# Kernel tuning notes

Measured on AMD Instinct MI355X. Metric: run time of the kernel, lower is better.

## Reference

```python
import jax, jax.numpy as jnp
import numpy as np

# MoE config (mirrors init_kwargs)
E = 8        # num_experts
K = 2        # num_experts_per_tok
H = 1024     # hidden_size
F = 2816     # moe_intermediate_size
B, S = 2, 512
NORM_TOPK = True


def setup_inputs() -> dict:
    key = jax.random.key(0)
    ks = jax.random.split(key, 5)
    x = jax.random.normal(ks[0], (B, S, H), dtype=jnp.float32)
    router_w = jax.random.normal(ks[1], (E, H), dtype=jnp.float32) * 0.02   # nn.Linear(H, E).weight
    gate_proj = jax.random.normal(ks[2], (E, H, F), dtype=jnp.float32) * 0.02
    up_proj = jax.random.normal(ks[3], (E, H, F), dtype=jnp.float32) * 0.02
    down_proj = jax.random.normal(ks[4], (E, F, H), dtype=jnp.float32) * 0.02
    return {"x": x, "router_w": router_w, "gate_proj": gate_proj,
            "up_proj": up_proj, "down_proj": down_proj}


def reference(x, router_w, gate_proj, up_proj, down_proj):
    b, s, h = x.shape
    xf = x.reshape(-1, h)                                    # [T, H]
    # Router: softmax over experts, top-k selection mask
    logits = xf @ router_w.T                                 # [T, E]
    probs = jax.nn.softmax(logits, axis=-1)
    topk_p, topk_i = jax.lax.top_k(probs, K)                 # [T, K]
    routing_map = jax.nn.one_hot(topk_i, E, dtype=probs.dtype).sum(axis=1)  # [T, E] 0/1
    if NORM_TOPK:
        probs = probs / topk_p.sum(-1, keepdims=True)
    weight = probs * routing_map                             # [T, E]; zero for unselected experts
    # Per-expert SwiGLU FFN; combine weighted by routing prob.
    # Dense-masked formulation: mathematically identical to the original
    # gather -> per-expert GEMM -> scatter_add, since weight==0 for unrouted pairs.
    g = jnp.einsum('th,ehf->tef', xf, gate_proj)             # [T, E, F]
    u = jnp.einsum('th,ehf->tef', xf, up_proj)               # [T, E, F]
    m = jax.nn.silu(g) * u                                   # [T, E, F]
    out = jnp.einsum('tef,efh,te->th', m, down_proj, weight) # [T, H]
    return out.reshape(b, s, h)
```

## Files before the change

kernel.cpp:

```cpp
#include <hip/hip_runtime.h>

#define HD 1024
#define FD 2816
#define NE 8
#define NT 1024
#define NSLOT (NT * 2)

typedef short short8 __attribute__((ext_vector_type(8)));
typedef short short4v __attribute__((ext_vector_type(4)));
typedef unsigned u32x4 __attribute__((ext_vector_type(4)));
typedef unsigned u32x2 __attribute__((ext_vector_type(2)));
typedef float f32x4 __attribute__((ext_vector_type(4)));
typedef float f32x16 __attribute__((ext_vector_type(16)));

typedef __attribute__((address_space(3))) unsigned lds_u32;
typedef __attribute__((address_space(1))) const unsigned glb_u32;

#define WAITV(N) asm volatile("s_waitcnt vmcnt(" #N ") lgkmcnt(0)" ::: "memory")
#define BARRIER() do { __builtin_amdgcn_s_barrier(); __builtin_amdgcn_sched_barrier(0); } while (0)

__device__ __forceinline__ void glds16(const void* g, void* l) {
  __builtin_amdgcn_global_load_lds((glb_u32*)g, (lds_u32*)l, 16, 0, 0);
}

__device__ __forceinline__ short f2bf(float f) {
  unsigned u = __builtin_bit_cast(unsigned, f);
  u += 0x7FFFu + ((u >> 16) & 1u);
  return (short)(u >> 16);
}

__device__ __forceinline__ unsigned cvtpk(float lo, float hi) {
  unsigned r;
  asm("v_cvt_pk_bf16_f32 %0, %1, %2" : "=v"(r) : "v"(lo), "v"(hi));
  return r;
}
__device__ __forceinline__ int imin(int a, int b) { return a < b ? a : b; }

__global__ void router_kernel(const float* __restrict__ x,
                              const float* __restrict__ rw,
                              int* __restrict__ counts,
                              int* __restrict__ tok_i,
                              float* __restrict__ tok_w) {
  const int t = blockIdx.x;
  const int lane = threadIdx.x;
  const float* px = x + (size_t)t * HD;
  float acc[NE];
#pragma unroll
  for (int e = 0; e < NE; e++) acc[e] = 0.f;
  for (int h = lane; h < HD; h += 64) {
    float xv = px[h];
#pragma unroll
    for (int e = 0; e < NE; e++) acc[e] += xv * rw[e * HD + h];
  }
#pragma unroll
  for (int e = 0; e < NE; e++) {
#pragma unroll
    for (int off = 32; off > 0; off >>= 1)
      acc[e] += __shfl_xor(acc[e], off, 64);
  }
  if (lane == 0) {
    float mx = acc[0];
#pragma unroll
    for (int e = 1; e < NE; e++) mx = fmaxf(mx, acc[e]);
    float ex[NE];
#pragma unroll
    for (int e = 0; e < NE; e++) ex[e] = __expf(acc[e] - mx);
    int i1 = 0;
#pragma unroll
    for (int e = 1; e < NE; e++) if (ex[e] > ex[i1]) i1 = e;
    int i2 = (i1 == 0) ? 1 : 0;
#pragma unroll
    for (int e = 0; e < NE; e++) if (e != i1 && ex[e] > ex[i2]) i2 = e;
    float inv = 1.f / (ex[i1] + ex[i2]);
    tok_i[t * 2 + 0] = i1; tok_w[t * 2 + 0] = ex[i1] * inv;
    tok_i[t * 2 + 1] = i2; tok_w[t * 2 + 1] = ex[i2] * inv;
    atomicAdd(&counts[i1], 1);
    atomicAdd(&counts[i2], 1);
  }
}

__global__ void scan_kernel(const int* __restrict__ counts,
                            int* __restrict__ bases,
                            int* __restrict__ cursor) {
  if (threadIdx.x == 0) {
    int s = 0;
    for (int e = 0; e < NE; e++) { bases[e] = s; cursor[e] = s; s += counts[e]; }
    bases[NE] = s;
  }
}

__global__ void fill_kernel(const int* __restrict__ tok_i,
                            const float* __restrict__ tok_w,
                            int* __restrict__ cursor,
                            int* __restrict__ slot_token,
                            float* __restrict__ slot_w,
                            int* __restrict__ slot_of) {
  int t = blockIdx.x * 256 + threadIdx.x;
  if (t >= NT) return;
#pragma unroll
  for (int k = 0; k < 2; k++) {
    int e = tok_i[t * 2 + k];
    int pos = atomicAdd(&cursor[e], 1);
    slot_token[pos] = t;
    slot_w[pos] = tok_w[t * 2 + k];
    slot_of[t * 2 + k] = pos;
  }
}

__global__ void gather_kernel(const float* __restrict__ x,
                              const int* __restrict__ slot_token,
                              short* __restrict__ xg) {
  const int slot = blockIdx.x;
  const int tok = slot_token[slot];
  const int t = threadIdx.x;
  f32x4 v = *(const f32x4*)(x + (size_t)tok * HD + t * 4);
  u32x2 s;
  s[0] = cvtpk(v[0], v[1]);
  s[1] = cvtpk(v[2], v[3]);
  *(u32x2*)&xg[(size_t)slot * HD + t * 4] = s;
}


#define GU_STAGEA(buf, k0) do {                                    \
    glds16(asrc[0] + (k0), &As[buf][wid * 512]);                   \
    glds16(asrc[1] + (k0), &As[buf][2048 + wid * 512]);            \
  } while (0)

#define GU_LOADB(G, U, k0) do {                                    \
    _Pragma("unroll")                                              \
    for (int ks = 0; ks < 2; ks++) {                               \
      _Pragma("unroll")                                            \
      for (int j = 0; j < 8; j++) {                                \
        unsigned idx = lidx + (unsigned)((k0) + ks * 16 + j) * FD; \
        G[ks * 8 + j] = Gw[idx];                                   \
        U[ks * 8 + j] = Uw[idx];                                   \
      }                                                            \
    }                                                              \
  } while (0)

#define GU_COMPUTE(Ab, G, U) do {                                             \
    _Pragma("unroll")                                                         \
    for (int ks = 0; ks < 2; ks++) {                                          \
      const int oct = ks * 2 + l5;                                            \
      short8 a0, a1;                                                          \
      { int r = wm * 64 + l31, p = r >> 1;                                    \
        a0 = *(const short8*)((Ab) + p * 64 +                                 \
              ((((r & 1) << 2) | oct) ^ (p & 7)) * 8); }                      \
      { int r = wm * 64 + 32 + l31, p = r >> 1;                               \
        a1 = *(const short8*)((Ab) + p * 64 +                                 \
              ((((r & 1) << 2) | oct) ^ (p & 7)) * 8); }                      \
      u32x4 ug, uu;                                                           \
      _Pragma("unroll")                                                       \
      for (int t2 = 0; t2 < 4; t2++) {                                        \
        ug[t2] = cvtpk(G[ks * 8 + 2 * t2], G[ks * 8 + 2 * t2 + 1]);           \
        uu[t2] = cvtpk(U[ks * 8 + 2 * t2], U[ks * 8 + 2 * t2 + 1]);           \
      }                                                                       \
      short8 bg = __builtin_bit_cast(short8, ug);                             \
      short8 bu = __builtin_bit_cast(short8, uu);                             \
      accG0 = __builtin_amdgcn_mfma_f32_32x32x16_bf16(a0, bg, accG0, 0, 0, 0);\
      accU0 = __builtin_amdgcn_mfma_f32_32x32x16_bf16(a0, bu, accU0, 0, 0, 0);\
      accG1 = __builtin_amdgcn_mfma_f32_32x32x16_bf16(a1, bg, accG1, 0, 0, 0);\
      accU1 = __builtin_amdgcn_mfma_f32_32x32x16_bf16(a1, bu, accU1, 0, 0, 0);\
    }                                                                         \
  } while (0)

__global__ __launch_bounds__(256, 2) void gateup_kernel(
    const short* __restrict__ xg, const float* __restrict__ gate_w,
    const float* __restrict__ up_w, const int* __restrict__ bases,
    short* __restrict__ m_out) {
  const int bx = blockIdx.x;
  const int e = bx / 44, nt = bx - e * 44;
  const int b0 = bases[e];
  const int ne = bases[e + 1] - b0;
  const int row0 = blockIdx.y * 128;
  if (row0 >= ne) return;
  const int n0 = nt * 64;

  __shared__ short As[2][4096];

  const int tid = threadIdx.x;
  const int lane = tid & 63, wid = tid >> 6;
  const int l31 = lane & 31, l5 = lane >> 5;
  const int wm = wid >> 1, wn = wid & 1;

  const short* asrc[2];
#pragma unroll
  for (int q = 0; q < 2; q++) {
    int i = q * 256 + tid;
    int p = i >> 3, j = i & 7;
    int v = j ^ (p & 7);
    int r = 2 * p + (v >> 2), c = v & 3;
    int slot = b0 + imin(row0 + r, ne - 1);
    asrc[q] = xg + (size_t)slot * HD + c * 8;
  }

  const float* Gw = gate_w + (size_t)e * HD * FD;
  const float* Uw = up_w + (size_t)e * HD * FD;
  const unsigned lidx = (unsigned)(l5 * 8) * FD + n0 + wn * 32 + l31;

  f32x16 accG0 = (f32x16)0.f, accG1 = (f32x16)0.f;
  f32x16 accU0 = (f32x16)0.f, accU1 = (f32x16)0.f;
  f32x16 bvAG, bvAU, bvBG, bvBU;

  GU_STAGEA(0, 0);
  __builtin_amdgcn_sched_barrier(0);
  GU_LOADB(bvAG, bvAU, 0);
  WAITV(32); BARRIER();

  for (int t = 0; t < 32; t += 2) {
    GU_STAGEA(1, (t + 1) * 32);
    __builtin_amdgcn_sched_barrier(0);
    GU_LOADB(bvBG, bvBU, (t + 1) * 32);
    GU_COMPUTE(&As[0][0], bvAG, bvAU);
    WAITV(32); BARRIER();
    if (t + 2 < 32) {
      GU_STAGEA(0, (t + 2) * 32);
      __builtin_amdgcn_sched_barrier(0);
      GU_LOADB(bvAG, bvAU, (t + 2) * 32);
      GU_COMPUTE(&As[1][0], bvBG, bvBU);
      WAITV(32); BARRIER();
    } else {
      GU_COMPUTE(&As[1][0], bvBG, bvBU);
    }
  }

#pragma unroll
  for (int q = 0; q < 16; q++) {
    int rb_ = (q & 3) + 8 * (q >> 2) + 4 * l5;
    {
      int r = row0 + wm * 64 + rb_;
      if (r < ne) {
        int slot = b0 + r;
        float g = accG0[q], u = accU0[q];
        float mv = (g / (1.f + __expf(-g))) * u;
        m_out[(size_t)slot * FD + n0 + wn * 32 + l31] = f2bf(mv);
      }
    }
    {
      int r = row0 + wm * 64 + 32 + rb_;
      if (r < ne) {
        int slot = b0 + r;
        float g = accG1[q], u = accU1[q];
        float mv = (g / (1.f + __expf(-g))) * u;
        m_out[(size_t)slot * FD + n0 + wn * 32 + l31] = f2bf(mv);
      }
    }
  }
}


#define DW_STAGEA(buf, k0) do {                                    \
    glds16(asrc[0] + (k0), &As[buf][wid * 512]);                   \
    glds16(asrc[1] + (k0), &As[buf][2048 + wid * 512]);            \
  } while (0)

#define DW_LOADB(B0, B1, k0) do {                                  \
    _Pragma("unroll")                                              \
    for (int ks = 0; ks < 4; ks++) {                               \
      _Pragma("unroll")                                            \
      for (int j = 0; j < 8; j++) {                                \
        unsigned idx = lidx + (unsigned)((k0) + ks * 16 + j) * HD; \
        if (ks < 2) B0[ks * 8 + j] = Dw[idx];                      \
        else        B1[(ks - 2) * 8 + j] = Dw[idx];                \
      }                                                            \
    }                                                              \
  } while (0)

#define DW_COMPUTE(Ab, B0, B1) do {                                           \
    _Pragma("unroll")                                                         \
    for (int ks = 0; ks < 4; ks++) {                                          \
      const int sub = ks >> 1, oct = (ks & 1) * 2 + l5;                       \
      int r = wm * 32 + l31, p = r >> 1;                                      \
      short8 a = *(const short8*)((Ab) + sub * 2048 + p * 64 +                \
                  ((((r & 1) << 2) | oct) ^ (p & 7)) * 8);                    \
      u32x4 ub;                                                               \
      _Pragma("unroll")                                                       \
      for (int t2 = 0; t2 < 4; t2++) {                                        \
        if (ks < 2)                                                           \
          ub[t2] = cvtpk(B0[ks * 8 + 2 * t2], B0[ks * 8 + 2 * t2 + 1]);       \
        else                                                                  \
          ub[t2] = cvtpk(B1[(ks - 2) * 8 + 2 * t2],                           \
                         B1[(ks - 2) * 8 + 2 * t2 + 1]);                      \
      }                                                                       \
      short8 bf = __builtin_bit_cast(short8, ub);                             \
      acc = __builtin_amdgcn_mfma_f32_32x32x16_bf16(a, bf, acc, 0, 0, 0);     \
    }                                                                         \
  } while (0)

__global__ __launch_bounds__(256, 3) void down_kernel(
    const short* __restrict__ m_in, const float* __restrict__ dw,
    const int* __restrict__ bases, const float* __restrict__ slot_w,
    float* __restrict__ out_slot) {
  const int bx = blockIdx.x;
  const int e = bx >> 4, nt = bx & 15;
  const int b0 = bases[e];
  const int ne = bases[e + 1] - b0;
  const int row0 = blockIdx.y * 64;
  if (row0 >= ne) return;
  const int n0 = nt * 64;

  __shared__ short As[2][4096];

  const int tid = threadIdx.x;
  const int lane = tid & 63, wid = tid >> 6;
  const int l31 = lane & 31, l5 = lane >> 5;
  const int wm = wid >> 1, wn = wid & 1;

  const short* asrc[2];
#pragma unroll
  for (int q = 0; q < 2; q++) {
    int i = q * 256 + tid;
    int sub = i >> 8, ci = i & 255;
    int p = ci >> 3, j = ci & 7;
    int v = j ^ (p & 7);
    int r = 2 * p + (v >> 2), c = v & 3;
    int slot = b0 + imin(row0 + r, ne - 1);
    asrc[q] = m_in + (size_t)slot * FD + sub * 32 + c * 8;
  }

  const float* Dw = dw + (size_t)e * FD * HD;
  const unsigned lidx = (unsigned)(l5 * 8) * HD + n0 + wn * 32 + l31;

  f32x16 acc = (f32x16)0.f;
  f32x16 bvA0, bvA1, bvB0, bvB1;

  DW_STAGEA(0, 0);
  __builtin_amdgcn_sched_barrier(0);
  DW_LOADB(bvA0, bvA1, 0);
  WAITV(32); BARRIER();

  const int NTL = FD / 64;
  for (int t = 0; t < NTL; t += 2) {
    DW_STAGEA(1, (t + 1) * 64);
    __builtin_amdgcn_sched_barrier(0);
    DW_LOADB(bvB0, bvB1, (t + 1) * 64);
    DW_COMPUTE(&As[0][0], bvA0, bvA1);
    WAITV(32); BARRIER();
    if (t + 2 < NTL) {
      DW_STAGEA(0, (t + 2) * 64);
      __builtin_amdgcn_sched_barrier(0);
      DW_LOADB(bvA0, bvA1, (t + 2) * 64);
      DW_COMPUTE(&As[1][0], bvB0, bvB1);
      WAITV(32); BARRIER();
    } else {
      DW_COMPUTE(&As[1][0], bvB0, bvB1);
    }
  }

#pragma unroll
  for (int q = 0; q < 16; q++) {
    int r = row0 + wm * 32 + (q & 3) + 8 * (q >> 2) + 4 * l5;
    if (r < ne) {
      int slot = b0 + r;
      out_slot[(size_t)slot * HD + n0 + wn * 32 + l31] = acc[q] * slot_w[slot];
    }
  }
}

__global__ void combine_kernel(const float* __restrict__ out_slot,
                               const int* __restrict__ slot_of,
                               float* __restrict__ out) {
  const int t = blockIdx.x;
  const int s0 = slot_of[t * 2];
  const int s1 = slot_of[t * 2 + 1];
  const int i = threadIdx.x * 4;
  f32x4 a = *(const f32x4*)(out_slot + (size_t)s0 * HD + i);
  f32x4 b = *(const f32x4*)(out_slot + (size_t)s1 * HD + i);
  f32x4 c = a + b;
  *(f32x4*)(out + (size_t)t * HD + i) = c;
}

extern "C" void kernel_launch(void* const* d_in, const int* in_sizes, int n_in,
                              void* d_out, int out_size, void* d_ws,
                              size_t ws_size, hipStream_t stream) {
  const float* x = (const float*)d_in[0];
  const float* rw = (const float*)d_in[1];
  const float* gw = (const float*)d_in[2];
  const float* uw = (const float*)d_in[3];
  const float* dw = (const float*)d_in[4];
  float* out = (float*)d_out;

  char* ws = (char*)d_ws;
  int* counts = (int*)(ws + 0);
  int* cursor = (int*)(ws + 64);
  int* bases = (int*)(ws + 128);
  int* tok_i = (int*)(ws + 256);
  float* tok_w = (float*)(ws + 8448);
  int* slot_token = (int*)(ws + 16640);
  float* slot_w = (float*)(ws + 24832);
  int* slot_of = (int*)(ws + 33024);
  short* xg = (short*)(ws + 41216);
  short* m_buf = (short*)(ws + 4235520);
  float* out_slot = (float*)(ws + 15769856);

  (void)hipMemsetAsync(counts, 0, 64, stream);
  router_kernel<<<NT, 64, 0, stream>>>(x, rw, counts, tok_i, tok_w);
  scan_kernel<<<1, 64, 0, stream>>>(counts, bases, cursor);
  fill_kernel<<<NT / 256, 256, 0, stream>>>(tok_i, tok_w, cursor, slot_token,
                                            slot_w, slot_of);
  gather_kernel<<<NSLOT, 256, 0, stream>>>(x, slot_token, xg);
  gateup_kernel<<<dim3(352, 16), 256, 0, stream>>>(xg, gw, uw, bases, m_buf);
  down_kernel<<<dim3(128, 32), 256, 0, stream>>>(m_buf, dw, bases, slot_w,
                                                 out_slot);
  combine_kernel<<<NT, 256, 0, stream>>>(out_slot, slot_of, out);
}
```

Before: 214.6 us.

## Deepen gate-up and down GEMM pipelines to three-stage prefetch

Both the gate/up and down GEMM kernels move from a double-buffered loop to a triple-buffered one, with three LDS A-stages and three register sets for B. Loads for step t+3 are issued right after computing step t, and the vmcnt waits are relaxed so more global loads stay in flight. The down kernel also cuts its K step from 64 to 32, which halves the per-stage LDS and register footprint. The cost is more live registers in gate/up (six f32x16 B buffers), which could cause spills or lower occupancy, and more barriers per unit of K in the down kernel.

```diff
diff --git a/kernel.cpp b/kernel.cpp
--- a/kernel.cpp
+++ b/kernel.cpp
@@ -7,7 +7,6 @@
 #define NSLOT (NT * 2)
 
 typedef short short8 __attribute__((ext_vector_type(8)));
-typedef short short4v __attribute__((ext_vector_type(4)));
 typedef unsigned u32x4 __attribute__((ext_vector_type(4)));
 typedef unsigned u32x2 __attribute__((ext_vector_type(2)));
 typedef float f32x4 __attribute__((ext_vector_type(4)));
@@ -18,6 +17,7 @@
 
 #define WAITV(N) asm volatile("s_waitcnt vmcnt(" #N ") lgkmcnt(0)" ::: "memory")
 #define BARRIER() do { __builtin_amdgcn_s_barrier(); __builtin_amdgcn_sched_barrier(0); } while (0)
+#define SB() __builtin_amdgcn_sched_barrier(0)
 
 __device__ __forceinline__ void glds16(const void* g, void* l) {
   __builtin_amdgcn_global_load_lds((glb_u32*)g, (lds_u32*)l, 16, 0, 0);
@@ -121,9 +121,9 @@
 }
 
 
-#define GU_STAGEA(buf, k0) do {                                    \
-    glds16(asrc[0] + (k0), &As[buf][wid * 512]);                   \
-    glds16(asrc[1] + (k0), &As[buf][2048 + wid * 512]);            \
+#define GU_STAGEA(S, koff) do {                                    \
+    glds16(asrc[0] + (koff), &As[S][wid * 512]);                   \
+    glds16(asrc[1] + (koff), &As[S][2048 + wid * 512]);            \
   } while (0)
 
 #define GU_LOADB(G, U, k0) do {                                    \
@@ -164,6 +164,16 @@
     }                                                                         \
   } while (0)
 
+#define GU_ITER(S, T) do {                       \
+    GU_COMPUTE(&As[S][0], bG##S, bU##S);         \
+    BARRIER();                                   \
+    GU_STAGEA(S, ((T) + 3) * 32);                \
+    SB();                                        \
+    GU_LOADB(bG##S, bU##S, ((T) + 3) * 32);      \
+    WAITV(63);                                   \
+    BARRIER();                                   \
+  } while (0)
+
 __global__ __launch_bounds__(256, 2) void gateup_kernel(
     const short* __restrict__ xg, const float* __restrict__ gate_w,
     const float* __restrict__ up_w, const int* __restrict__ bases,
@@ -176,7 +186,7 @@
   if (row0 >= ne) return;
   const int n0 = nt * 64;
 
-  __shared__ short As[2][4096];
+  __shared__ short As[3][4096];
 
   const int tid = threadIdx.x;
   const int lane = tid & 63, wid = tid >> 6;
@@ -200,29 +210,26 @@
 
   f32x16 accG0 = (f32x16)0.f, accG1 = (f32x16)0.f;
   f32x16 accU0 = (f32x16)0.f, accU1 = (f32x16)0.f;
-  f32x16 bvAG, bvAU, bvBG, bvBU;
-
-  GU_STAGEA(0, 0);
-  __builtin_amdgcn_sched_barrier(0);
-  GU_LOADB(bvAG, bvAU, 0);
-  WAITV(32); BARRIER();
-
-  for (int t = 0; t < 32; t += 2) {
-    GU_STAGEA(1, (t + 1) * 32);
-    __builtin_amdgcn_sched_barrier(0);
-    GU_LOADB(bvBG, bvBU, (t + 1) * 32);
-    GU_COMPUTE(&As[0][0], bvAG, bvAU);
-    WAITV(32); BARRIER();
-    if (t + 2 < 32) {
-      GU_STAGEA(0, (t + 2) * 32);
-      __builtin_amdgcn_sched_barrier(0);
-      GU_LOADB(bvAG, bvAU, (t + 2) * 32);
-      GU_COMPUTE(&As[1][0], bvBG, bvBU);
-      WAITV(32); BARRIER();
-    } else {
-      GU_COMPUTE(&As[1][0], bvBG, bvBU);
-    }
-  }
+  f32x16 bG0, bU0, bG1, bU1, bG2, bU2;
+
+  GU_STAGEA(0, 0);  SB(); GU_LOADB(bG0, bU0, 0);  SB();
+  GU_STAGEA(1, 32); SB(); GU_LOADB(bG1, bU1, 32); SB();
+  GU_STAGEA(2, 64); SB(); GU_LOADB(bG2, bU2, 64);
+  WAITV(63);
+  BARRIER();
+
+  for (int t = 0; t < 27; t += 3) {
+    GU_ITER(0, t);
+    GU_ITER(1, t + 1);
+    GU_ITER(2, t + 2);
+  }
+  GU_ITER(0, 27);
+  GU_ITER(1, 28);
+  GU_COMPUTE(&As[2][0], bG2, bU2);
+  WAITV(34); BARRIER();
+  GU_COMPUTE(&As[0][0], bG0, bU0);
+  WAITV(0); BARRIER();
+  GU_COMPUTE(&As[1][0], bG1, bU1);
 
 #pragma unroll
   for (int q = 0; q < 16; q++) {
@@ -249,42 +256,43 @@
 }
 
 
-#define DW_STAGEA(buf, k0) do {                                    \
-    glds16(asrc[0] + (k0), &As[buf][wid * 512]);                   \
-    glds16(asrc[1] + (k0), &As[buf][2048 + wid * 512]);            \
-  } while (0)
-
-#define DW_LOADB(B0, B1, k0) do {                                  \
+#define DW_STAGEA(S, koff) glds16(asrc + (koff), &As[S][wid * 512])
+
+#define DW_LOADB(B, k0) do {                                       \
     _Pragma("unroll")                                              \
-    for (int ks = 0; ks < 4; ks++) {                               \
+    for (int ks = 0; ks < 2; ks++) {                               \
       _Pragma("unroll")                                            \
       for (int j = 0; j < 8; j++) {                                \
         unsigned idx = lidx + (unsigned)((k0) + ks * 16 + j) * HD; \
-        if (ks < 2) B0[ks * 8 + j] = Dw[idx];                      \
-        else        B1[(ks - 2) * 8 + j] = Dw[idx];                \
+        B[ks * 8 + j] = Dw[idx];                                   \
       }                                                            \
     }                                                              \
   } while (0)
 
-#define DW_COMPUTE(Ab, B0, B1) do {                                           \
+#define DW_COMPUTE(Ab, B) do {                                                \
     _Pragma("unroll")                                                         \
-    for (int ks = 0; ks < 4; ks++) {                                          \
-      const int sub = ks >> 1, oct = (ks & 1) * 2 + l5;                       \
+    for (int ks = 0; ks < 2; ks++) {                                          \
+      const int oct = ks * 2 + l5;                                            \
       int r = wm * 32 + l31, p = r >> 1;                                      \
-      short8 a = *(const short8*)((Ab) + sub * 2048 + p * 64 +                \
+      short8 a = *(const short8*)((Ab) + p * 64 +                             \
                   ((((r & 1) << 2) | oct) ^ (p & 7)) * 8);                    \
       u32x4 ub;                                                               \
       _Pragma("unroll")                                                       \
-      for (int t2 = 0; t2 < 4; t2++) {                                        \
-        if (ks < 2)                                                           \
-          ub[t2] = cvtpk(B0[ks * 8 + 2 * t2], B0[ks * 8 + 2 * t2 + 1]);       \
-        else                                                                  \
-          ub[t2] = cvtpk(B1[(ks - 2) * 8 + 2 * t2],                           \
-                         B1[(ks - 2) * 8 + 2 * t2 + 1]);                      \
-      }                                                                       \
+      for (int t2 = 0; t2 < 4; t2++)                                          \
+        ub[t2] = cvtpk(B[ks * 8 + 2 * t2], B[ks * 8 + 2 * t2 + 1]);           \
       short8 bf = __builtin_bit_cast(short8, ub);                             \
       acc = __builtin_amdgcn_mfma_f32_32x32x16_bf16(a, bf, acc, 0, 0, 0);     \
     }                                                                         \
+  } while (0)
+
+#define DW_ITER(S, T) do {                       \
+    DW_COMPUTE(&As[S][0], bv##S);                \
+    BARRIER();                                   \
+    DW_STAGEA(S, ((T) + 3) * 32);                \
+    SB();                                        \
+    DW_LOADB(bv##S, ((T) + 3) * 32);             \
+    WAITV(34);                                   \
+    BARRIER();                                   \
   } while (0)
 
 __global__ __launch_bounds__(256, 3) void down_kernel(
@@ -299,53 +307,45 @@
   if (row0 >= ne) return;
   const int n0 = nt * 64;
 
-  __shared__ short As[2][4096];
+  __shared__ short As[3][2048];
 
   const int tid = threadIdx.x;
   const int lane = tid & 63, wid = tid >> 6;
   const int l31 = lane & 31, l5 = lane >> 5;
   const int wm = wid >> 1, wn = wid & 1;
 
-  const short* asrc[2];
-#pragma unroll
-  for (int q = 0; q < 2; q++) {
-    int i = q * 256 + tid;
-    int sub = i >> 8, ci = i & 255;
-    int p = ci >> 3, j = ci & 7;
+  const short* asrc;
+  {
+    int p = tid >> 3, j = tid & 7;
     int v = j ^ (p & 7);
     int r = 2 * p + (v >> 2), c = v & 3;
     int slot = b0 + imin(row0 + r, ne - 1);
-    asrc[q] = m_in + (size_t)slot * FD + sub * 32 + c * 8;
+    asrc = m_in + (size_t)slot * FD + c * 8;
   }
 
   const float* Dw = dw + (size_t)e * FD * HD;
   const unsigned lidx = (unsigned)(l5 * 8) * HD + n0 + wn * 32 + l31;
 
   f32x16 acc = (f32x16)0.f;
-  f32x16 bvA0, bvA1, bvB0, bvB1;
-
-  DW_STAGEA(0, 0);
-  __builtin_amdgcn_sched_barrier(0);
-  DW_LOADB(bvA0, bvA1, 0);
-  WAITV(32); BARRIER();
-
-  const int NTL = FD / 64;
-  for (int t = 0; t < NTL; t += 2) {
-    DW_STAGEA(1, (t + 1) * 64);
-    __builtin_amdgcn_sched_barrier(0);
-    DW_LOADB(bvB0, bvB1, (t + 1) * 64);
-    DW_COMPUTE(&As[0][0], bvA0, bvA1);
-    WAITV(32); BARRIER();
-    if (t + 2 < NTL) {
-      DW_STAGEA(0, (t + 2) * 64);
-      __builtin_amdgcn_sched_barrier(0);
-      DW_LOADB(bvA0, bvA1, (t + 2) * 64);
-      DW_COMPUTE(&As[1][0], bvB0, bvB1);
-      WAITV(32); BARRIER();
-    } else {
-      DW_COMPUTE(&As[1][0], bvB0, bvB1);
-    }
-  }
+  f32x16 bv0, bv1, bv2;
+
+  DW_STAGEA(0, 0);  SB(); DW_LOADB(bv0, 0);  SB();
+  DW_STAGEA(1, 32); SB(); DW_LOADB(bv1, 32); SB();
+  DW_STAGEA(2, 64); SB(); DW_LOADB(bv2, 64);
+  WAITV(34);
+  BARRIER();
+
+  for (int t = 0; t < 84; t += 3) {
+    DW_ITER(0, t);
+    DW_ITER(1, t + 1);
+    DW_ITER(2, t + 2);
+  }
+  DW_ITER(0, 84);
+  DW_COMPUTE(&As[1][0], bv1);
+  WAITV(17); BARRIER();
+  DW_COMPUTE(&As[2][0], bv2);
+  WAITV(0); BARRIER();
+  DW_COMPUTE(&As[0][0], bv0);
 
 #pragma unroll
   for (int q = 0; q < 16; q++) {
```

Result: faster. 203.9 us (-5.0%).
